# Performance work log

Measured on AMD Instinct MI355X. Metric: run time of the kernel, lower is better.

Reference implementation:

```python
import jax, jax.numpy as jnp
import numpy as np

T_SIM = 32  # simulation_length


def _uniform_spikes(rates, cycle, T):
    """Port of to_uniform_spikes: place round(rate*T) evenly spaced spikes over T cycles."""
    Ns = jnp.round(rates * T).astype(jnp.int32)
    mask = (Ns != 0) & (Ns != T) & (cycle < T)
    N_safe = jnp.maximum(Ns, 1)
    spacing = T / N_safe.astype(rates.dtype)
    cyc = jnp.asarray(cycle, rates.dtype)
    res = mask & (jnp.floor(cyc / spacing) < N_safe.astype(rates.dtype)) & (jnp.floor(jnp.mod(cyc, spacing)) == 0)
    res = res.astype(rates.dtype)
    return jnp.where(Ns == T, jnp.asarray(1.0, rates.dtype), res)


def setup_inputs() -> dict:
    key = jax.random.key(0)
    k1, k2 = jax.random.split(key)
    B, N, C = 256, 2048, 8
    x = jax.random.uniform(k1, (B, N), dtype=jnp.float32)          # preprocessed rates in [0,1]
    W = jax.random.normal(k2, (C, N, N), dtype=jnp.float32) * 0.02  # core_matrix per core, (n_in, n_out)
    thresholds = jnp.ones((C,), dtype=jnp.float32)
    return {"x": x, "W": W, "thresholds": thresholds}


def reference(x, W, thresholds):
    """Spiking simulation of a chain of C cores over T cycles.

    Core c has latency c; core 0 reads input spikes, core c reads core c-1's
    previous-cycle buffer; output counts accumulate the last core's buffer.
    """
    T = T_SIM
    dtype = x.dtype
    B, N = x.shape
    C = W.shape[0]
    lat = jnp.arange(C)  # per-core pipeline latency (chain topology)

    # input spike train (T, B, N), padded with (C-1) zero cycles (post-T input is zeros)
    train = jax.vmap(lambda c: _uniform_spikes(x, c, T))(jnp.arange(T))
    train = jnp.concatenate([train, jnp.zeros((C - 1, B, N), dtype)], axis=0)

    thr = thresholds[:, None, None]  # (C,1,1)

    def step(carry, input_spikes):
        memb, buf, counts, cycle = carry
        # gather phase: all cores read prior-cycle buffers / current input spikes
        signals = jnp.concatenate([input_spikes[None], buf[:-1]], axis=0)  # (C,B,N)
        active = (cycle >= lat) & (cycle < T + lat)  # (C,)
        am = active[:, None, None]
        # integrate: memb += signals @ core_matrix (only for active cores)
        delta = jnp.einsum('cbi,cio->cbo', signals, W)
        memb2 = memb + jnp.where(am, delta, jnp.asarray(0.0, dtype))
        # fire: thresholding_mode '<'  ->  fired = (threshold < memb)
        fired = thr < memb2
        buf2 = jnp.where(am, fired.astype(dtype), buf)
        # firing_mode 'Default': subtract threshold from fired membranes
        memb3 = jnp.where(am & fired, memb2 - thr, memb2)
        counts2 = counts + buf2[-1]  # output spans = last core's full buffer
        return (memb3, buf2, counts2, cycle + 1), None

    init = (jnp.zeros((C, B, N), dtype),
            jnp.zeros((C, B, N), dtype),
            jnp.zeros((B, N), dtype),
            jnp.int32(0))
    (_, _, counts, _), _ = jax.lax.scan(step, init, train)
    # spike counts -> rates
    return counts / T
```

## Files before the change

### kernel.cpp

```cpp
#include <hip/hip_runtime.h>
#include <stdint.h>

#define NN 2048
#define NCORE 8
#define TSIM 32
#define PLANE (256*2048)

typedef int i4v __attribute__((ext_vector_type(4)));

__device__ __forceinline__ void load_lds16(const void* g, void* l) {
  __builtin_amdgcn_global_load_lds((const __attribute__((address_space(1))) void*)g,
                                   (__attribute__((address_space(3))) void*)l, 16, 0, 0);
}

__global__ void spikes_kernel(const float* __restrict__ x, uint8_t* __restrict__ strain) {
  int gid = blockIdx.x * 256 + threadIdx.x;
  int b = gid >> 7, kg = gid & 127;
  const float* xp = x + (size_t)b * NN + kg * 16;
  float nsf[16], sp[16]; int ns[16];
#pragma unroll
  for (int e = 0; e < 16; ++e) {
    float nv = rintf(xp[e] * 32.0f);
    nsf[e] = nv; ns[e] = (int)nv; sp[e] = 32.0f / fmaxf(nv, 1.0f);
  }
  uint32_t dst = (uint32_t)b * 2048 + ((uint32_t)(kg >> 2) << 6)
               + ((uint32_t)((kg & 3) ^ ((b >> 1) & 3)) << 4);
  int cyc0 = blockIdx.y * 4;
#pragma unroll
  for (int i = 0; i < 4; ++i) {
    int cyc = cyc0 + i;
    float ct = (float)cyc;
    uint32_t w[4] = {0u, 0u, 0u, 0u};
#pragma unroll
    for (int e = 0; e < 16; ++e) {
      bool res;
      if (ns[e] == TSIM)      res = true;
      else if (ns[e] == 0)    res = false;
      else {
        float q = floorf(ct / sp[e]);
        float m = fmodf(ct, sp[e]);
        res = (q < nsf[e]) && (floorf(m) == 0.0f);
      }
      if (res) w[e >> 2] |= 1u << ((e & 3) * 8);
    }
    uint4 pk; pk.x = w[0]; pk.y = w[1]; pk.z = w[2]; pk.w = w[3];
    *(uint4*)(strain + (size_t)cyc * PLANE + dst) = pk;
  }
}

__global__ __launch_bounds__(256) void wsplit_kernel(const float* __restrict__ W,
                                                     uint8_t* __restrict__ Whm) {
  __shared__ uint32_t lds[3 * 2048];
  int kk = blockIdx.x, nt = blockIdx.y, c = blockIdx.z;
  int tid = threadIdx.x, lane = tid & 63, wid = tid >> 6;
  const float* src = W + ((size_t)c * NN + (size_t)kk * 128) * NN + nt * 64 + lane;
#pragma unroll
  for (int kp = 0; kp < 8; ++kp) {
    uint32_t pk0 = 0, pk1 = 0, pk2 = 0;
#pragma unroll
    for (int q = 0; q < 4; ++q) {
      int kl = kp * 16 + wid * 4 + q;
      float w = src[(size_t)kl * NN];
      int wi = (int)rintf(w * 0x1p25f);
      int l8 = (int)(int8_t)(uint8_t)(wi & 0xFF);
      int r1 = (wi - l8) >> 8;
      int m8 = (int)(int8_t)(uint8_t)(r1 & 0xFF);
      int h8 = (r1 - m8) >> 8;
      pk0 |= ((uint32_t)(uint8_t)h8) << (q * 8);
      pk1 |= ((uint32_t)(uint8_t)m8) << (q * 8);
      pk2 |= ((uint32_t)(uint8_t)l8) << (q * 8);
    }
    int kq = kp * 4 + wid;
    lds[0 * 2048 + kq * 64 + lane] = pk0;
    lds[1 * 2048 + kq * 64 + lane] = pk1;
    lds[2 * 2048 + kq * 64 + lane] = pk2;
  }
  __syncthreads();
  size_t chunkbase = (((size_t)c * 32 + nt) * 16 + kk) * 24576;
#pragma unroll
  for (int g = 0; g < 6; ++g) {
    int idx = g * 256 + tid;
    int ks2 = (idx >= 768) ? 1 : 0;
    int rem = idx - ks2 * 768;
    int p = rem >> 8;
    int n = (rem >> 2) & 63;
    int s = rem & 3;
    int k16 = s ^ ((n >> 1) & 3);
    int kqb = ks2 * 16 + k16 * 4;
    uint4 v;
    v.x = lds[p * 2048 + (kqb + 0) * 64 + n];
    v.y = lds[p * 2048 + (kqb + 1) * 64 + n];
    v.z = lds[p * 2048 + (kqb + 2) * 64 + n];
    v.w = lds[p * 2048 + (kqb + 3) * 64 + n];
    *(uint4*)(Whm + chunkbase + (size_t)idx * 16) = v;
  }
}

__global__ __launch_bounds__(512, 4) void step8_kernel(
    const uint8_t* __restrict__ Whm, const float* __restrict__ thresholds,
    const uint8_t* __restrict__ strain, uint8_t* bufs,
    float* __restrict__ memb, float* __restrict__ out, int j, int c_lo) {
  __shared__ uint8_t smem[77824];

  const int tid = threadIdx.x;
  const int c = c_lo + blockIdx.x;
  const int yy = blockIdx.y;
  const int nt64 = yy >> 3, nh = (yy >> 2) & 1, rq = yy & 3;
  const int sl = 8 * (j - c);
  const int l = tid & 63, wid = tid >> 6;
  const int wm = wid >> 1, wn = wid & 1;
  const int lr = l & 15, lh = l >> 4;
  uint8_t* Bs = smem + 65536;

  const uint8_t* srcb = (c == 0) ? strain : bufs + (size_t)(c - 1) * 16 * PLANE;
  const uint8_t* ab[4];
  uint32_t adst[4];
#pragma unroll
  for (int j_ = 0; j_ < 4; ++j_) {
    int gi = j_ * 512 + tid;
    int si = gi >> 8, idx = gi & 255;
    int row = idx >> 2, kq = idx & 3;
    int pid = (c == 0) ? (sl + si) : ((sl + si) & 15);
    ab[j_] = srcb + (size_t)pid * PLANE + (size_t)(rq * 64 + row) * 2048 + kq * 16;
    adst[j_] = si * 8192 + idx * 16;
  }
  const uint8_t* bb = Whm + (((size_t)c * 32 + nt64) * 16) * 24576
                    + ((size_t)(tid >> 7) * 256 + (size_t)nh * 128 + (tid & 127)) * 16;

  const uint32_t swz = (uint32_t)(lh ^ ((lr >> 1) & 3)) << 4;
  const uint32_t aoff = (uint32_t)(wm * 16 + lr) * 64 + swz;
  const uint32_t boff = (uint32_t)(wn * 16 + lr) * 64 + swz;

  i4v acc[8][3];
  const i4v izero = {0, 0, 0, 0};
#pragma unroll
  for (int st = 0; st < 8; ++st)
#pragma unroll
    for (int p = 0; p < 3; ++p) acc[st][p] = izero;

  auto issue = [&](int k, int slot) {
#pragma unroll
    for (int j_ = 0; j_ < 4; ++j_)
      load_lds16(ab[j_] + k * 64, smem + adst[j_] + slot * 4096);
    if (tid < 384)
      load_lds16(bb + (size_t)(k >> 1) * 24576 + (size_t)(k & 1) * 12288,
                 Bs + slot * 6144 + tid * 16);
  };

  auto comp = [&](int slot) {
    const uint8_t* Bb = Bs + slot * 6144;
    i4v bf0 = *(const i4v*)(Bb + 0 * 2048 + boff);
    i4v bf1 = *(const i4v*)(Bb + 1 * 2048 + boff);
    i4v bf2 = *(const i4v*)(Bb + 2 * 2048 + boff);
    __builtin_amdgcn_s_setprio(1);
#pragma unroll
    for (int st = 0; st < 8; ++st) {
      i4v a_ = *(const i4v*)(smem + st * 8192 + slot * 4096 + aoff);
      acc[st][0] = __builtin_amdgcn_mfma_i32_16x16x64_i8(a_, bf0, acc[st][0], 0, 0, 0);
      acc[st][1] = __builtin_amdgcn_mfma_i32_16x16x64_i8(a_, bf1, acc[st][1], 0, 0, 0);
      acc[st][2] = __builtin_amdgcn_mfma_i32_16x16x64_i8(a_, bf2, acc[st][2], 0, 0, 0);
    }
    __builtin_amdgcn_s_setprio(0);
  };

#define WAITV(n) asm volatile("s_waitcnt vmcnt(" #n ")" ::: "memory")
#define WAITL() asm volatile("s_waitcnt lgkmcnt(0)" ::: "memory")
#define BAR() do { __builtin_amdgcn_s_barrier(); __builtin_amdgcn_sched_barrier(0); } while (0)

  issue(0, 0);
  for (int k = 0; k < 32; ++k) {
    if (k < 31) {
      issue(k + 1, (k + 1) & 1);
      if (wid < 6) { WAITV(5); } else { WAITV(4); }
    } else {
      WAITV(0);
    }
    BAR();
    comp(k & 1);
    WAITL();
    BAR();
  }
#undef WAITV
#undef WAITL
#undef BAR

  const float thr = thresholds[c];
  float* Cl = (float*)smem;
  const int err = tid >> 3;
  const int ec4 = (tid & 7) * 4;
  float4 d[8];
#pragma unroll
  for (int st = 0; st < 8; ++st) {
    __syncthreads();
#pragma unroll
    for (int rg = 0; rg < 4; ++rg) {
      int row = wm * 16 + lh * 4 + rg;
      int col = wn * 16 + lr;
      int di = (acc[st][0][rg] << 16) + (acc[st][1][rg] << 8) + acc[st][2][rg];
      Cl[row * 36 + col] = (float)di * 0x1p-25f;
    }
    __syncthreads();
    d[st] = *(const float4*)&Cl[err * 36 + ec4];
  }

  const int b = rq * 64 + err;
  const int o = nt64 * 64 + nh * 32 + ec4;
  const size_t idx = (size_t)b * NN + o;
  float* membp = memb + (size_t)c * PLANE;
  float4 mv;
  if (j == c) mv = make_float4(0.f, 0.f, 0.f, 0.f);
  else        mv = *(float4*)(membp + idx);
  float4 cv;
  if (c == 7) {
    if (j == 7) cv = make_float4(0.f, 0.f, 0.f, 0.f);
    else        cv = *(float4*)(out + idx);
  }
  const uint32_t ba = (uint32_t)b * 2048 + ((uint32_t)(o >> 6) << 6)
                    + ((uint32_t)(((o >> 4) & 3) ^ ((b >> 1) & 3)) << 4) + (o & 15);
#pragma unroll
  for (int st = 0; st < 8; ++st) {
    mv.x += d[st].x; mv.y += d[st].y; mv.z += d[st].z; mv.w += d[st].w;
    bool fx = thr < mv.x, fy = thr < mv.y, fz = thr < mv.z, fw = thr < mv.w;
    if (fx) mv.x -= thr;  if (fy) mv.y -= thr;
    if (fz) mv.z -= thr;  if (fw) mv.w -= thr;
    if (c < 7) {
      uint8_t* bpl = bufs + ((size_t)c * 16 + ((sl + st) & 15)) * PLANE;
      uchar4 pk;
      pk.x = fx ? 1 : 0; pk.y = fy ? 1 : 0; pk.z = fz ? 1 : 0; pk.w = fw ? 1 : 0;
      *(uchar4*)(bpl + ba) = pk;
    } else {
      cv.x += fx ? 1.f : 0.f; cv.y += fy ? 1.f : 0.f;
      cv.z += fz ? 1.f : 0.f; cv.w += fw ? 1.f : 0.f;
    }
  }
  *(float4*)(membp + idx) = mv;
  if (c == 7) {
    if (j == 10) { cv.x *= 0x1p-5f; cv.y *= 0x1p-5f; cv.z *= 0x1p-5f; cv.w *= 0x1p-5f; }
    *(float4*)(out + idx) = cv;
  }
}

extern "C" void kernel_launch(void* const* d_in, const int* in_sizes, int n_in,
                              void* d_out, int out_size, void* d_ws, size_t ws_size,
                              hipStream_t stream) {
  const float* x   = (const float*)d_in[0];
  const float* W   = (const float*)d_in[1];
  const float* thr = (const float*)d_in[2];
  float* out = (float*)d_out;
  uint8_t* ws = (uint8_t*)d_ws;

  float*   memb   = (float*)ws;
  uint8_t* strain = ws + 16777216;
  uint8_t* bufs   = ws + 33554432;
  uint8_t* Whm    = ws + 92274688;

  spikes_kernel<<<dim3(128, 8), 256, 0, stream>>>(x, strain);
  wsplit_kernel<<<dim3(16, 32, 8), 256, 0, stream>>>(W, Whm);

  for (int j = 0; j < 11; ++j) {
    int c_lo = (j > 3) ? (j - 3) : 0;
    int c_hi = (j < 7) ? j : 7;
    step8_kernel<<<dim3(c_hi - c_lo + 1, 256), 512, 0, stream>>>(
        Whm, thr, strain, bufs, memb, out, j, c_lo);
  }
}
```

Baseline: 966.6 us.

## Process four timesteps per launch with smaller tiles and more wavefronts

Each chain-step kernel now handles 4 simulation cycles per core instead of 8. The schedule grows from 11 to 15 wavefront launches, and the spike ring buffer shrinks to 8 planes per core. Tiles change to 32 rows × 64 outputs with a 2×4 warp layout, and LDS drops to 40KB with launch bounds raised to 8 blocks. The aim is better occupancy and a shorter pipeline fill. In exchange, weights are reloaded more often per timestep and there are more kernel launches.

```diff
diff --git a/kernel.cpp b/kernel.cpp
--- a/kernel.cpp
+++ b/kernel.cpp
@@ -96,66 +96,62 @@
   }
 }
 
-__global__ __launch_bounds__(512, 4) void step8_kernel(
+__global__ __launch_bounds__(512, 8) void step4_kernel(
     const uint8_t* __restrict__ Whm, const float* __restrict__ thresholds,
     const uint8_t* __restrict__ strain, uint8_t* bufs,
     float* __restrict__ memb, float* __restrict__ out, int j, int c_lo) {
-  __shared__ uint8_t smem[77824];
+  __shared__ uint8_t smem[40960];
 
   const int tid = threadIdx.x;
   const int c = c_lo + blockIdx.x;
   const int yy = blockIdx.y;
-  const int nt64 = yy >> 3, nh = (yy >> 2) & 1, rq = yy & 3;
-  const int sl = 8 * (j - c);
+  const int nt = yy >> 3, rq = yy & 7;
+  const int sl = 4 * (j - c);
   const int l = tid & 63, wid = tid >> 6;
-  const int wm = wid >> 1, wn = wid & 1;
+  const int wm = wid >> 2, wn = wid & 3;
   const int lr = l & 15, lh = l >> 4;
-  uint8_t* Bs = smem + 65536;
-
-  const uint8_t* srcb = (c == 0) ? strain : bufs + (size_t)(c - 1) * 16 * PLANE;
-  const uint8_t* ab[4];
-  uint32_t adst[4];
-#pragma unroll
-  for (int j_ = 0; j_ < 4; ++j_) {
-    int gi = j_ * 512 + tid;
-    int si = gi >> 8, idx = gi & 255;
-    int row = idx >> 2, kq = idx & 3;
-    int pid = (c == 0) ? (sl + si) : ((sl + si) & 15);
-    ab[j_] = srcb + (size_t)pid * PLANE + (size_t)(rq * 64 + row) * 2048 + kq * 16;
-    adst[j_] = si * 8192 + idx * 16;
-  }
-  const uint8_t* bb = Whm + (((size_t)c * 32 + nt64) * 16) * 24576
-                    + ((size_t)(tid >> 7) * 256 + (size_t)nh * 128 + (tid & 127)) * 16;
+
+  const uint8_t* pls[4];
+#pragma unroll
+  for (int st = 0; st < 4; ++st)
+    pls[st] = (c == 0) ? strain + (size_t)(sl + st) * PLANE
+                       : bufs + ((size_t)(c - 1) * 8 + ((sl + st) & 7)) * PLANE;
+
+  const int asi = tid >> 7, aidx = tid & 127;
+  const uint8_t* ab = pls[asi] + (size_t)(rq * 32 + (aidx >> 2)) * 2048 + (aidx & 3) * 16;
+  const uint32_t adst = (uint32_t)asi * 4096 + (uint32_t)aidx * 16;
+  const uint8_t* wbase = Whm + (((size_t)c * 32 + nt) * 16) * 24576;
+  uint8_t* Bs = smem + 16384;
 
   const uint32_t swz = (uint32_t)(lh ^ ((lr >> 1) & 3)) << 4;
   const uint32_t aoff = (uint32_t)(wm * 16 + lr) * 64 + swz;
   const uint32_t boff = (uint32_t)(wn * 16 + lr) * 64 + swz;
 
-  i4v acc[8][3];
+  i4v acc[4][3];
   const i4v izero = {0, 0, 0, 0};
 #pragma unroll
-  for (int st = 0; st < 8; ++st)
+  for (int st = 0; st < 4; ++st)
 #pragma unroll
     for (int p = 0; p < 3; ++p) acc[st][p] = izero;
 
   auto issue = [&](int k, int slot) {
-#pragma unroll
-    for (int j_ = 0; j_ < 4; ++j_)
-      load_lds16(ab[j_] + k * 64, smem + adst[j_] + slot * 4096);
-    if (tid < 384)
-      load_lds16(bb + (size_t)(k >> 1) * 24576 + (size_t)(k & 1) * 12288,
-                 Bs + slot * 6144 + tid * 16);
+    load_lds16(ab + k * 64, smem + adst + slot * 2048);
+    const uint8_t* bs = wbase + (size_t)(k >> 1) * 24576 + (size_t)(k & 1) * 12288;
+    uint8_t* Bd = Bs + slot * 12288;
+    load_lds16(bs + tid * 16, Bd + tid * 16);
+    if (tid < 256) load_lds16(bs + 8192 + tid * 16, Bd + 8192 + tid * 16);
   };
 
   auto comp = [&](int slot) {
-    const uint8_t* Bb = Bs + slot * 6144;
-    i4v bf0 = *(const i4v*)(Bb + 0 * 2048 + boff);
-    i4v bf1 = *(const i4v*)(Bb + 1 * 2048 + boff);
-    i4v bf2 = *(const i4v*)(Bb + 2 * 2048 + boff);
+    const uint8_t* Bb = Bs + slot * 12288;
+    i4v bf0 = *(const i4v*)(Bb + 0 * 4096 + boff);
+    i4v bf1 = *(const i4v*)(Bb + 1 * 4096 + boff);
+    i4v bf2 = *(const i4v*)(Bb + 2 * 4096 + boff);
+    const uint8_t* Ab = smem + slot * 2048;
     __builtin_amdgcn_s_setprio(1);
 #pragma unroll
-    for (int st = 0; st < 8; ++st) {
-      i4v a_ = *(const i4v*)(smem + st * 8192 + slot * 4096 + aoff);
+    for (int st = 0; st < 4; ++st) {
+      i4v a_ = *(const i4v*)(Ab + st * 4096 + aoff);
       acc[st][0] = __builtin_amdgcn_mfma_i32_16x16x64_i8(a_, bf0, acc[st][0], 0, 0, 0);
       acc[st][1] = __builtin_amdgcn_mfma_i32_16x16x64_i8(a_, bf1, acc[st][1], 0, 0, 0);
       acc[st][2] = __builtin_amdgcn_mfma_i32_16x16x64_i8(a_, bf2, acc[st][2], 0, 0, 0);
@@ -171,7 +167,7 @@
   for (int k = 0; k < 32; ++k) {
     if (k < 31) {
       issue(k + 1, (k + 1) & 1);
-      if (wid < 6) { WAITV(5); } else { WAITV(4); }
+      if (tid < 256) { WAITV(3); } else { WAITV(2); }
     } else {
       WAITV(0);
     }
@@ -186,25 +182,23 @@
 
   const float thr = thresholds[c];
   float* Cl = (float*)smem;
-  const int err = tid >> 3;
-  const int ec4 = (tid & 7) * 4;
-  float4 d[8];
-#pragma unroll
-  for (int st = 0; st < 8; ++st) {
+  float4 d[4];
+#pragma unroll
+  for (int st = 0; st < 4; ++st) {
     __syncthreads();
 #pragma unroll
     for (int rg = 0; rg < 4; ++rg) {
       int row = wm * 16 + lh * 4 + rg;
       int col = wn * 16 + lr;
       int di = (acc[st][0][rg] << 16) + (acc[st][1][rg] << 8) + acc[st][2][rg];
-      Cl[row * 36 + col] = (float)di * 0x1p-25f;
+      Cl[row * 68 + col] = (float)di * 0x1p-25f;
     }
     __syncthreads();
-    d[st] = *(const float4*)&Cl[err * 36 + ec4];
-  }
-
-  const int b = rq * 64 + err;
-  const int o = nt64 * 64 + nh * 32 + ec4;
+    d[st] = *(const float4*)&Cl[(tid >> 4) * 68 + (tid & 15) * 4];
+  }
+
+  const int b = rq * 32 + (tid >> 4);
+  const int o = nt * 64 + (tid & 15) * 4;
   const size_t idx = (size_t)b * NN + o;
   float* membp = memb + (size_t)c * PLANE;
   float4 mv;
@@ -218,13 +212,13 @@
   const uint32_t ba = (uint32_t)b * 2048 + ((uint32_t)(o >> 6) << 6)
                     + ((uint32_t)(((o >> 4) & 3) ^ ((b >> 1) & 3)) << 4) + (o & 15);
 #pragma unroll
-  for (int st = 0; st < 8; ++st) {
+  for (int st = 0; st < 4; ++st) {
     mv.x += d[st].x; mv.y += d[st].y; mv.z += d[st].z; mv.w += d[st].w;
     bool fx = thr < mv.x, fy = thr < mv.y, fz = thr < mv.z, fw = thr < mv.w;
     if (fx) mv.x -= thr;  if (fy) mv.y -= thr;
     if (fz) mv.z -= thr;  if (fw) mv.w -= thr;
     if (c < 7) {
-      uint8_t* bpl = bufs + ((size_t)c * 16 + ((sl + st) & 15)) * PLANE;
+      uint8_t* bpl = bufs + ((size_t)c * 8 + ((sl + st) & 7)) * PLANE;
       uchar4 pk;
       pk.x = fx ? 1 : 0; pk.y = fy ? 1 : 0; pk.z = fz ? 1 : 0; pk.w = fw ? 1 : 0;
       *(uchar4*)(bpl + ba) = pk;
@@ -235,7 +229,7 @@
   }
   *(float4*)(membp + idx) = mv;
   if (c == 7) {
-    if (j == 10) { cv.x *= 0x1p-5f; cv.y *= 0x1p-5f; cv.z *= 0x1p-5f; cv.w *= 0x1p-5f; }
+    if (j == 14) { cv.x *= 0x1p-5f; cv.y *= 0x1p-5f; cv.z *= 0x1p-5f; cv.w *= 0x1p-5f; }
     *(float4*)(out + idx) = cv;
   }
 }
@@ -252,15 +246,15 @@
   float*   memb   = (float*)ws;
   uint8_t* strain = ws + 16777216;
   uint8_t* bufs   = ws + 33554432;
-  uint8_t* Whm    = ws + 92274688;
+  uint8_t* Whm    = ws + 62914560;
 
   spikes_kernel<<<dim3(128, 8), 256, 0, stream>>>(x, strain);
   wsplit_kernel<<<dim3(16, 32, 8), 256, 0, stream>>>(W, Whm);
 
-  for (int j = 0; j < 11; ++j) {
-    int c_lo = (j > 3) ? (j - 3) : 0;
+  for (int j = 0; j < 15; ++j) {
+    int c_lo = (j > 7) ? (j - 7) : 0;
     int c_hi = (j < 7) ? j : 7;
-    step8_kernel<<<dim3(c_hi - c_lo + 1, 256), 512, 0, stream>>>(
+    step4_kernel<<<dim3(c_hi - c_lo + 1, 256), 512, 0, stream>>>(
         Whm, thr, strain, bufs, memb, out, j, c_lo);
   }
 }
```

Measured after the change: 3.673 ms. +280.0%, slower.
